# Kernel optimization log

Hardware: AMD Instinct MI355X
Metric: run time of the kernel (lower is better)

## Reference

```python
import jax, jax.numpy as jnp
import numpy as np

EMBED_DIM = 768
EMBED_PER_TYPE = EMBED_DIM // 6  # 128


def setup_inputs() -> dict:
    key = jax.random.key(0)
    ks = jax.random.split(key, 6)
    d = EMBED_PER_TYPE
    return {
        "price_w": jax.random.normal(ks[0], (1, d), dtype=jnp.float32),
        "size_w": jax.random.normal(ks[1], (1, d), dtype=jnp.float32),
        "exchange_w": jax.random.normal(ks[2], (4, d), dtype=jnp.float32),
        "pair_w": jax.random.normal(ks[3], (8, d), dtype=jnp.float32),
        "level_w": jax.random.normal(ks[4], (16, d), dtype=jnp.float32),
        "time_w": jax.random.normal(ks[5], (32, d), dtype=jnp.float32),
        "num_features": 131072,
    }


def reference(price_w, size_w, exchange_w, pair_w, level_w, time_w, num_features):
    # Vectorized version of the per-feature loop: indices are 0, 0, i%3, i%7, i%15, i%31.
    idx = jnp.arange(num_features)
    parts = [
        jnp.broadcast_to(price_w[0], (num_features, EMBED_PER_TYPE)),
        jnp.broadcast_to(size_w[0], (num_features, EMBED_PER_TYPE)),
        exchange_w[idx % 3],
        pair_w[idx % 7],
        level_w[idx % 15],
        time_w[idx % 31],
    ]
    return jnp.concatenate(parts, axis=-1)  # [num_features, embed_dim]
```

## Files before the change

kernel.cpp:

```cpp
#include <hip/hip_runtime.h>

#define ROW_F4 192
#define CHUNK  16
#define ROWS_PER_BLOCK (4 * CHUNK)

typedef float v4f __attribute__((ext_vector_type(4)));

template <bool NT>
__global__ __launch_bounds__(256) void smart_embedding_kernel(
    const v4f* __restrict__ price_w,
    const v4f* __restrict__ size_w,
    const v4f* __restrict__ exchange_w,
    const v4f* __restrict__ pair_w,
    const v4f* __restrict__ level_w,
    const v4f* __restrict__ time_w,
    v4f* __restrict__ out,
    int row0,
    int rows_end)
{
    const int tid  = threadIdx.x;
    const int wave = tid >> 6;
    const int lane = tid & 63;
    const int off  = lane & 31;
    const bool hi  = lane >= 32;

    int r0 = row0 + (blockIdx.x * 4 + wave) * CHUNK;
    if (r0 >= rows_end) return;
    const int rend = (r0 + CHUNK < rows_end) ? r0 + CHUNK : rows_end;

    const v4f v0 = hi ? size_w[off] : price_w[off];

    const v4f* base1 = hi ? pair_w : exchange_w;
    const v4f* base2 = hi ? time_w : level_w;
    const int p1 = hi ? 7  : 3;
    const int p2 = hi ? 31 : 15;

    int m1 = r0 % p1;
    int m2 = r0 % p2;

    v4f* orow = out + (size_t)r0 * ROW_F4 + lane;

#pragma unroll 4
    for (int r = r0; r < rend; ++r) {
        v4f v1 = base1[m1 * 32 + off];
        v4f v2 = base2[m2 * 32 + off];
        if constexpr (NT) {
            __builtin_nontemporal_store(v0, orow);
            __builtin_nontemporal_store(v1, orow + 64);
            __builtin_nontemporal_store(v2, orow + 128);
        } else {
            orow[0]   = v0;
            orow[64]  = v1;
            orow[128] = v2;
        }
        orow += ROW_F4;
        m1 = (m1 + 1 == p1) ? 0 : m1 + 1;
        m2 = (m2 + 1 == p2) ? 0 : m2 + 1;
    }
}

static inline void launch_seg(bool nt, const v4f* price_w, const v4f* size_w,
                              const v4f* exchange_w, const v4f* pair_w,
                              const v4f* level_w, const v4f* time_w,
                              v4f* out, int row0, int rows_end, hipStream_t stream) {
    if (rows_end <= row0) return;
    const int blocks = (rows_end - row0 + ROWS_PER_BLOCK - 1) / ROWS_PER_BLOCK;
    if (nt)
        smart_embedding_kernel<true><<<blocks, 256, 0, stream>>>(
            price_w, size_w, exchange_w, pair_w, level_w, time_w, out, row0, rows_end);
    else
        smart_embedding_kernel<false><<<blocks, 256, 0, stream>>>(
            price_w, size_w, exchange_w, pair_w, level_w, time_w, out, row0, rows_end);
}

extern "C" void kernel_launch(void* const* d_in, const int* in_sizes, int n_in,
                              void* d_out, int out_size, void* d_ws, size_t ws_size,
                              hipStream_t stream) {
    const v4f* price_w    = (const v4f*)d_in[0];
    const v4f* size_w     = (const v4f*)d_in[1];
    const v4f* exchange_w = (const v4f*)d_in[2];
    const v4f* pair_w     = (const v4f*)d_in[3];
    const v4f* level_w    = (const v4f*)d_in[4];
    const v4f* time_w     = (const v4f*)d_in[5];
    v4f* out = (v4f*)d_out;

    const int rows = out_size / 768;

    int q = (rows / 4) & ~(ROWS_PER_BLOCK - 1);
    int b0 = q, b1 = 2 * q, b2 = 3 * q;

    launch_seg(true,  price_w, size_w, exchange_w, pair_w, level_w, time_w, out, 0,   b0,   stream);
    launch_seg(false, price_w, size_w, exchange_w, pair_w, level_w, time_w, out, b0,  b1,   stream);
    launch_seg(true,  price_w, size_w, exchange_w, pair_w, level_w, time_w, out, b1,  b2,   stream);
    launch_seg(false, price_w, size_w, exchange_w, pair_w, level_w, time_w, out, b2,  rows, stream);
}
```

Before: 412.8 us.

## Assign each wave a residue class of the index period and stride rows

Each wave now owns one residue class modulo lcm(3,7,15,31)=3255. It loads its three embedding vectors once and writes them to every row in that class, striding by 3255 rows. This removes the per-row table loads and modulo updates. It also replaces the four-segment launch that alternated non-temporal and normal stores with a single launch using normal stores. The cost is strided, scattered writes across rows instead of contiguous chunks, and a grid of only about 814 blocks.

```diff
diff --git a/kernel.cpp b/kernel.cpp
--- a/kernel.cpp
+++ b/kernel.cpp
@@ -1,12 +1,10 @@
 #include <hip/hip_runtime.h>
 
 #define ROW_F4 192
-#define CHUNK  16
-#define ROWS_PER_BLOCK (4 * CHUNK)
+#define NCLS   3255
 
 typedef float v4f __attribute__((ext_vector_type(4)));
 
-template <bool NT>
 __global__ __launch_bounds__(256) void smart_embedding_kernel(
     const v4f* __restrict__ price_w,
     const v4f* __restrict__ size_w,
@@ -15,8 +13,7 @@
     const v4f* __restrict__ level_w,
     const v4f* __restrict__ time_w,
     v4f* __restrict__ out,
-    int row0,
-    int rows_end)
+    int rows)
 {
     const int tid  = threadIdx.x;
     const int wave = tid >> 6;
@@ -24,53 +21,25 @@
     const int off  = lane & 31;
     const bool hi  = lane >= 32;
 
-    int r0 = row0 + (blockIdx.x * 4 + wave) * CHUNK;
-    if (r0 >= rows_end) return;
-    const int rend = (r0 + CHUNK < rows_end) ? r0 + CHUNK : rows_end;
+    const int cls = blockIdx.x * 4 + wave;
+    if (cls >= NCLS) return;
 
     const v4f v0 = hi ? size_w[off] : price_w[off];
+    const int m1 = hi ? cls % 7  : cls % 3;
+    const int m2 = hi ? cls % 31 : cls % 15;
+    const v4f v1 = (hi ? pair_w     : exchange_w)[m1 * 32 + off];
+    const v4f v2 = (hi ? time_w     : level_w  )[m2 * 32 + off];
 
-    const v4f* base1 = hi ? pair_w : exchange_w;
-    const v4f* base2 = hi ? time_w : level_w;
-    const int p1 = hi ? 7  : 3;
-    const int p2 = hi ? 31 : 15;
-
-    int m1 = r0 % p1;
-    int m2 = r0 % p2;
-
-    v4f* orow = out + (size_t)r0 * ROW_F4 + lane;
+    v4f* orow = out + (size_t)cls * ROW_F4 + lane;
+    const size_t step = (size_t)NCLS * ROW_F4;
 
 #pragma unroll 4
-    for (int r = r0; r < rend; ++r) {
-        v4f v1 = base1[m1 * 32 + off];
-        v4f v2 = base2[m2 * 32 + off];
-        if constexpr (NT) {
-            __builtin_nontemporal_store(v0, orow);
-            __builtin_nontemporal_store(v1, orow + 64);
-            __builtin_nontemporal_store(v2, orow + 128);
-        } else {
-            orow[0]   = v0;
-            orow[64]  = v1;
-            orow[128] = v2;
-        }
-        orow += ROW_F4;
-        m1 = (m1 + 1 == p1) ? 0 : m1 + 1;
-        m2 = (m2 + 1 == p2) ? 0 : m2 + 1;
+    for (int r = cls; r < rows; r += NCLS) {
+        orow[0]   = v0;
+        orow[64]  = v1;
+        orow[128] = v2;
+        orow += step;
     }
-}
-
-static inline void launch_seg(bool nt, const v4f* price_w, const v4f* size_w,
-                              const v4f* exchange_w, const v4f* pair_w,
-                              const v4f* level_w, const v4f* time_w,
-                              v4f* out, int row0, int rows_end, hipStream_t stream) {
-    if (rows_end <= row0) return;
-    const int blocks = (rows_end - row0 + ROWS_PER_BLOCK - 1) / ROWS_PER_BLOCK;
-    if (nt)
-        smart_embedding_kernel<true><<<blocks, 256, 0, stream>>>(
-            price_w, size_w, exchange_w, pair_w, level_w, time_w, out, row0, rows_end);
-    else
-        smart_embedding_kernel<false><<<blocks, 256, 0, stream>>>(
-            price_w, size_w, exchange_w, pair_w, level_w, time_w, out, row0, rows_end);
 }
 
 extern "C" void kernel_launch(void* const* d_in, const int* in_sizes, int n_in,
@@ -85,12 +54,8 @@
     v4f* out = (v4f*)d_out;
 
     const int rows = out_size / 768;
+    const int blocks = (NCLS + 3) / 4;
 
-    int q = (rows / 4) & ~(ROWS_PER_BLOCK - 1);
-    int b0 = q, b1 = 2 * q, b2 = 3 * q;
-
-    launch_seg(true,  price_w, size_w, exchange_w, pair_w, level_w, time_w, out, 0,   b0,   stream);
-    launch_seg(false, price_w, size_w, exchange_w, pair_w, level_w, time_w, out, b0,  b1,   stream);
-    launch_seg(true,  price_w, size_w, exchange_w, pair_w, level_w, time_w, out, b1,  b2,   stream);
-    launch_seg(false, price_w, size_w, exchange_w, pair_w, level_w, time_w, out, b2,  rows, stream);
+    smart_embedding_kernel<<<blocks, 256, 0, stream>>>(
+        price_w, size_w, exchange_w, pair_w, level_w, time_w, out, rows);
 }
```

Result: no change. 407.0 us (-1.4%).
